# Kernel optimization log

Hardware: AMD Instinct MI355X
Metric: run time of the kernel (lower is better)

Reference implementation:

```python
import jax, jax.numpy as jnp
import numpy as np
import math


def _selective_scan(u, delta, A, Bs, Cs, D, delta_bias):
    """Mamba selective scan.
    u, delta: (B,K,Dn,L); A: (K,Dn,N); Bs, Cs: (B,K,N,L); D, delta_bias: (K,Dn).
    delta_softplus=True semantics from selective_scan_fn.
    """
    delta = jax.nn.softplus(delta + delta_bias[None, :, :, None])
    dl = jnp.moveaxis(delta, -1, 0)  # (L,B,K,Dn)
    ul = jnp.moveaxis(u, -1, 0)      # (L,B,K,Dn)
    bl = jnp.moveaxis(Bs, -1, 0)     # (L,B,K,N)
    cl = jnp.moveaxis(Cs, -1, 0)     # (L,B,K,N)
    h0 = jnp.zeros(u.shape[:3] + (A.shape[-1],), u.dtype)  # (B,K,Dn,N)

    def step(h, inp):
        d, ut, bt, ct = inp
        h = jnp.exp(d[..., None] * A) * h + (d * ut)[..., None] * bt[:, :, None, :]
        y = jnp.einsum('bkdn,bkn->bkd', h, ct)
        return h, y

    _, ys = jax.lax.scan(step, h0, (dl, ul, bl, cl))
    return jnp.moveaxis(ys, 0, -1) + D[None, :, :, None] * u  # (B,K,Dn,L)


def setup_inputs() -> dict:
    key = jax.random.key(0)
    B, H, W, C = 8, 64, 64, 192
    Dn, N, R, K = 192, 8, 12, 4
    ks = jax.random.split(key, 8)
    x = jax.random.normal(ks[0], (B, H, W, C), jnp.float32)
    in_proj_w = jax.random.normal(ks[1], (2 * Dn, C), jnp.float32) * (C ** -0.5)
    conv_w = jax.random.normal(ks[2], (Dn, 1, 3, 3), jnp.float32) * 0.2
    conv_b = jnp.zeros((Dn,), jnp.float32)
    x_proj_w = jax.random.normal(ks[3], (K, R + 2 * N, Dn), jnp.float32) * (Dn ** -0.5)
    dt_std = R ** -0.5
    dt_projs_w = jax.random.uniform(ks[4], (K, Dn, R), jnp.float32, -dt_std, dt_std)
    dt = jnp.exp(jax.random.uniform(ks[5], (K, Dn), jnp.float32)
                 * (math.log(0.1) - math.log(0.001)) + math.log(0.001))
    dt = jnp.clip(dt, 1e-4, None)
    dt_projs_b = dt + jnp.log(-jnp.expm1(-dt))  # inverse softplus
    A_logs = jnp.broadcast_to(jnp.log(jnp.arange(1, N + 1, dtype=jnp.float32)), (K, Dn, N)).copy()
    Ds = jnp.ones((K, Dn), jnp.float32)
    ln_w = jnp.ones((Dn,), jnp.float32)
    ln_b = jnp.zeros((Dn,), jnp.float32)
    out_proj_w = jax.random.normal(ks[6], (C, Dn), jnp.float32) * (Dn ** -0.5)
    return {"x": x, "in_proj_w": in_proj_w, "conv_w": conv_w, "conv_b": conv_b,
            "x_proj_w": x_proj_w, "dt_projs_w": dt_projs_w, "dt_projs_b": dt_projs_b,
            "A_logs": A_logs, "Ds": Ds, "ln_w": ln_w, "ln_b": ln_b,
            "out_proj_w": out_proj_w}


def reference(x, in_proj_w, conv_w, conv_b, x_proj_w, dt_projs_w, dt_projs_b,
              A_logs, Ds, ln_w, ln_b, out_proj_w):
    B, H, W, C = x.shape
    K, _, Dn = x_proj_w.shape
    N = A_logs.shape[-1]
    R = dt_projs_w.shape[-1]
    L = H * W

    xz = x @ in_proj_w.T                       # (B,H,W,2*Dn)
    xf, z = jnp.split(xz, 2, axis=-1)
    xc = jnp.transpose(xf, (0, 3, 1, 2))       # (B,Dn,H,W)
    xc = jax.lax.conv_general_dilated(
        xc, conv_w, (1, 1), [(1, 1), (1, 1)],
        feature_group_count=Dn,
        dimension_numbers=('NCHW', 'OIHW', 'NCHW')) + conv_b[None, :, None, None]
    xc = jax.nn.silu(xc)

    # 4-directional scan sequences: hw, wh, reversed-hw, reversed-wh
    x_hw = xc.reshape(B, Dn, L)
    x_wh = jnp.transpose(xc, (0, 1, 3, 2)).reshape(B, Dn, L)
    x2 = jnp.stack([x_hw, x_wh], axis=1)
    xs = jnp.concatenate([x2, jnp.flip(x2, axis=-1)], axis=1)  # (B,4,Dn,L)

    x_dbl = jnp.einsum('bkdl,kcd->bkcl', xs, x_proj_w)
    dts, Bsx, Csx = jnp.split(x_dbl, [R, R + N], axis=2)
    dts = jnp.einsum('bkrl,kdr->bkdl', dts, dt_projs_w)

    A = -jnp.exp(A_logs)                       # (K,Dn,N)
    out_y = _selective_scan(xs, dts, A, Bsx, Csx, Ds, dt_projs_b)  # (B,4,Dn,L)

    inv_y = jnp.flip(out_y[:, 2:4], axis=-1)
    wh_y = jnp.transpose(out_y[:, 1].reshape(B, Dn, W, H), (0, 1, 3, 2)).reshape(B, Dn, L)
    invwh_y = jnp.transpose(inv_y[:, 1].reshape(B, Dn, W, H), (0, 1, 3, 2)).reshape(B, Dn, L)
    y = out_y[:, 0] + inv_y[:, 0] + wh_y + invwh_y  # (B,Dn,L)

    y = jnp.transpose(y, (0, 2, 1)).reshape(B, H, W, Dn)
    mu = y.mean(-1, keepdims=True)
    var = y.var(-1, keepdims=True)
    y = (y - mu) / jnp.sqrt(var + 1e-5) * ln_w + ln_b
    y = y * jax.nn.silu(z)
    return y @ out_proj_w.T
```

## Files before the change

### kernel.cpp

```cpp
#include <hip/hip_runtime.h>
#include <hip/hip_bf16.h>

constexpr int B_  = 8;
constexpr int H_  = 64;
constexpr int W_  = 64;
constexpr int C_  = 192;
constexpr int Dn  = 192;
constexpr int Nst = 8;
constexpr int R_  = 12;
constexpr int K_  = 4;
constexpr int L_  = H_ * W_;
constexpr int CS  = 32;
constexpr int GS  = 8;
constexpr int NC  = L_ / CS;
constexpr int CPROJ = R_ + 2 * Nst;
constexpr int MROWS = B_ * L_;

typedef __attribute__((ext_vector_type(8))) short short8v;
typedef __attribute__((ext_vector_type(4))) float f32x4;
typedef __attribute__((ext_vector_type(2))) float f32x2;

__device__ __forceinline__ int map_t(int k, int t) {
    int tt = (k >= 2) ? (L_ - 1 - t) : t;
    if (k & 1) tt = (tt & 63) * 64 + (tt >> 6);
    return tt;
}

__device__ __forceinline__ short f2bf(float f) {
    unsigned u = __float_as_uint(f);
    u += 0x7FFFu + ((u >> 16) & 1u);
    return (short)(u >> 16);
}
__device__ __forceinline__ float bf2f(short s) {
    return __uint_as_float(((unsigned)(unsigned short)s) << 16);
}

__device__ __forceinline__ f32x2 mk2(float a, float b) { f32x2 v; v.x = a; v.y = b; return v; }
__device__ __forceinline__ f32x2 lo2(float4 v) { return mk2(v.x, v.y); }
__device__ __forceinline__ f32x2 hi2(float4 v) { return mk2(v.z, v.w); }
__device__ __forceinline__ f32x2 pkfma(f32x2 a, f32x2 b, f32x2 c) {
    return __builtin_elementwise_fma(a, b, c);
}

constexpr int WOFF_IN  = 0;
constexpr int WOFF_XP  = 73728;
constexpr int WOFF_OUT = 95232;
constexpr int WTOTAL   = 132096;
constexpr int XUNITS   = MROWS * Dn / 8;
constexpr int WUNITS   = WTOTAL / 8;
__global__ __launch_bounds__(256) void k_cvt(const float* __restrict__ x,
                                             const float* __restrict__ w_in,
                                             const float* __restrict__ xpw,
                                             const float* __restrict__ wout,
                                             short* __restrict__ x_bf,
                                             short* __restrict__ w_bf) {
    int g = blockIdx.x * 256 + threadIdx.x;
    const float* src;
    short* dst;
    int off;
    if (g < XUNITS) { src = x; dst = x_bf; off = g * 8; }
    else {
        g -= XUNITS;
        if (g >= WUNITS) return;
        int base = g * 8;
        dst = w_bf; off = base;
        if (base < WOFF_XP)       { src = w_in; }
        else if (base < WOFF_OUT) { src = xpw;  src -= WOFF_XP; }
        else                      { src = wout; src -= WOFF_OUT; }
    }
    float4 a = *reinterpret_cast<const float4*>(src + off);
    float4 b = *reinterpret_cast<const float4*>(src + off + 4);
    short8v v = {f2bf(a.x), f2bf(a.y), f2bf(a.z), f2bf(a.w),
                 f2bf(b.x), f2bf(b.y), f2bf(b.z), f2bf(b.w)};
    *reinterpret_cast<short8v*>(dst + off) = v;
}

__device__ __forceinline__ void mgemm_core(const short* __restrict__ A,
                                           const short* __restrict__ Wb,
                                           f32x4 (&acc)[4][2],
                                           int mrow, int ncol, int Nact, int K) {
    const int lane = threadIdx.x & 63;
    const int koff = (lane >> 4) * 8;
    for (int k0 = 0; k0 < K; k0 += 32) {
        short8v af[4], bfr[2];
#pragma unroll
        for (int mf = 0; mf < 4; mf++)
            af[mf] = *reinterpret_cast<const short8v*>(
                A + (size_t)(mrow + mf * 16) * K + k0 + koff);
#pragma unroll
        for (int nf = 0; nf < 2; nf++) {
            int r = ncol + nf * 16;
            short8v z = {0, 0, 0, 0, 0, 0, 0, 0};
            bfr[nf] = (r < Nact)
                ? *reinterpret_cast<const short8v*>(Wb + (size_t)r * K + k0 + koff)
                : z;
        }
#pragma unroll
        for (int mf = 0; mf < 4; mf++)
#pragma unroll
            for (int nf = 0; nf < 2; nf++)
                acc[mf][nf] = __builtin_amdgcn_mfma_f32_16x16x32_bf16(
                    af[mf], bfr[nf], acc[mf][nf], 0, 0, 0);
    }
}

__global__ __launch_bounds__(256) void k_mgemm_f(const short* __restrict__ A,
                                                 const short* __restrict__ Wb,
                                                 float* __restrict__ out0,
                                                 int Nact, int K) {
    const int m0 = blockIdx.x * 128, n0 = blockIdx.y * 64;
    const int wid = threadIdx.x >> 6, lane = threadIdx.x & 63;
    const int wm = wid >> 1, wn = wid & 1;
    f32x4 acc[4][2] = {};
    mgemm_core(A, Wb, acc, m0 + wm * 64 + (lane & 15), n0 + wn * 32 + (lane & 15),
               Nact, K);
    const int prow = (lane >> 4) * 4, pcol = lane & 15;
#pragma unroll
    for (int mf = 0; mf < 4; mf++) {
        int mbase = m0 + wm * 64 + mf * 16 + prow;
#pragma unroll
        for (int nf = 0; nf < 2; nf++) {
            int n = n0 + wn * 32 + nf * 16 + pcol;
            if (n >= Nact) continue;
#pragma unroll
            for (int r = 0; r < 4; r++)
                out0[(size_t)(mbase + r) * Nact + n] = acc[mf][nf][r];
        }
    }
}

__global__ __launch_bounds__(256) void k_mgemm_in(const short* __restrict__ A,
                                                  const short* __restrict__ Wb,
                                                  short* __restrict__ xf_bf,
                                                  short* __restrict__ z_bf,
                                                  int K) {
    const int m0 = blockIdx.x * 128, n0 = blockIdx.y * 64;
    const int wid = threadIdx.x >> 6, lane = threadIdx.x & 63;
    const int wm = wid >> 1, wn = wid & 1;
    f32x4 acc[4][2] = {};
    mgemm_core(A, Wb, acc, m0 + wm * 64 + (lane & 15), n0 + wn * 32 + (lane & 15),
               384, K);
    const int prow = (lane >> 4) * 4, pcol = lane & 15;
#pragma unroll
    for (int mf = 0; mf < 4; mf++) {
        int mbase = m0 + wm * 64 + mf * 16 + prow;
#pragma unroll
        for (int nf = 0; nf < 2; nf++) {
            int n = n0 + wn * 32 + nf * 16 + pcol;
#pragma unroll
            for (int r = 0; r < 4; r++) {
                int m = mbase + r;
                if (n < 192) xf_bf[(size_t)m * 192 + n] = f2bf(acc[mf][nf][r]);
                else         z_bf[(size_t)m * 192 + (n - 192)] = f2bf(acc[mf][nf][r]);
            }
        }
    }
}

__global__ __launch_bounds__(192) void k_conv(const short* __restrict__ xfb,
                                              const float* __restrict__ cw,
                                              const float* __restrict__ cb,
                                              short* __restrict__ xcb) {
    const int tid = threadIdx.x;
    const int dg = tid % 48;
    const int wl = tid / 48;
    const int blk = blockIdx.x;
    const int wq = blk & 15;
    const int hq = (blk >> 4) & 7;
    const int b  = blk >> 7;
    const int w  = wq * 4 + wl;
    const int d  = dg * 4;
    const int h0 = hq * 8;

    short4 win[3][10];
    const short4 z4 = make_short4(0, 0, 0, 0);
#pragma unroll
    for (int kw = 0; kw < 3; kw++) {
        int ww = w + kw - 1;
        bool wok = (unsigned)ww < (unsigned)W_;
        int wc = min(max(ww, 0), W_ - 1);
#pragma unroll
        for (int r = 0; r < 10; r++) {
            int hh = h0 - 1 + r;
            bool ok = wok && ((unsigned)hh < (unsigned)H_);
            int hc = min(max(hh, 0), H_ - 1);
            short4 v = *reinterpret_cast<const short4*>(
                xfb + (((size_t)b * H_ + hc) * W_ + wc) * Dn + d);
            win[kw][r] = ok ? v : z4;
        }
    }

    float wgt[4][9];
    float bias[4];
#pragma unroll
    for (int c = 0; c < 4; c++) {
        bias[c] = cb[d + c];
#pragma unroll
        for (int t = 0; t < 9; t++) wgt[c][t] = cw[(d + c) * 9 + t];
    }

#pragma unroll
    for (int j = 0; j < 8; j++) {
        float a0 = bias[0], a1 = bias[1], a2 = bias[2], a3 = bias[3];
#pragma unroll
        for (int kh = 0; kh < 3; kh++)
#pragma unroll
            for (int kw = 0; kw < 3; kw++) {
                short4 v = win[kw][j + kh];
                int t = kh * 3 + kw;
                a0 = fmaf(bf2f(v.x), wgt[0][t], a0);
                a1 = fmaf(bf2f(v.y), wgt[1][t], a1);
                a2 = fmaf(bf2f(v.z), wgt[2][t], a2);
                a3 = fmaf(bf2f(v.w), wgt[3][t], a3);
            }
        short4 o;
        o.x = f2bf(a0 / (1.f + __expf(-a0)));
        o.y = f2bf(a1 / (1.f + __expf(-a1)));
        o.z = f2bf(a2 / (1.f + __expf(-a2)));
        o.w = f2bf(a3 / (1.f + __expf(-a3)));
        *reinterpret_cast<short4*>(
            xcb + (((size_t)b * H_ + h0 + j) * W_ + w) * Dn + d) = o;
    }
}

__device__ __forceinline__ void delta_e1(float x, float& delta, float& e1) {
    float t = __expf(fminf(x, 80.f));
    float opt = 1.f + t;
    delta = __logf(opt);
    e1 = __builtin_amdgcn_rcpf(opt);
}

__device__ __forceinline__ float dot12p(const float4& q0, const float4& q1,
                                        const float4& q2, const f32x2* w2,
                                        float bias) {
    f32x2 a0 = pkfma(lo2(q0), w2[0], mk2(bias, 0.f));
    f32x2 a1 = lo2(q1) * w2[2];
    a0 = pkfma(hi2(q0), w2[1], a0);
    a1 = pkfma(hi2(q1), w2[3], a1);
    a0 = pkfma(lo2(q2), w2[4], a0);
    a1 = pkfma(hi2(q2), w2[5], a1);
    f32x2 s = a0 + a1;
    return s.x + s.y;
}

__device__ __forceinline__ float dot12(const float4& a, const float4& b,
                                       const float4& c, const float* w, float x) {
    x = fmaf(a.x, w[0], x);  x = fmaf(a.y, w[1], x);
    x = fmaf(a.z, w[2], x);  x = fmaf(a.w, w[3], x);
    x = fmaf(b.x, w[4], x);  x = fmaf(b.y, w[5], x);
    x = fmaf(b.z, w[6], x);  x = fmaf(b.w, w[7], x);
    x = fmaf(c.x, w[8], x);  x = fmaf(c.y, w[9], x);
    x = fmaf(c.z, w[10], x); x = fmaf(c.w, w[11], x);
    return x;
}

__global__ __launch_bounds__(192, 4) void k_scan1(const short* __restrict__ xcb,
                                               const float* __restrict__ xdbl,
                                               const float* __restrict__ dtw_all,
                                               const float* __restrict__ dtb_all,
                                               const float* __restrict__ alog,
                                               float* __restrict__ Aprod,
                                               float* __restrict__ hpart) {
    const int blk = blockIdx.x;
    const int c = blk % NC;
    const int k = (blk / NC) % K_;
    const int b = blk / (NC * K_);
    const int d = threadIdx.x;
    const int t0 = c * CS;
    const int stride = ((k & 1) ? 64 : 1) * ((k >= 2) ? -1 : 1);
    const int lm0 = map_t(k, t0);

    __shared__ float4 sx4[CS][5];
    const float4* xd4 = reinterpret_cast<const float4*>(xdbl);
    for (int i = d; i < CS * 5; i += 192) {
        int ts = i / 5, q = i % 5;
        sx4[ts][q] = xd4[((size_t)b * L_ + lm0 + ts * stride) * 28 + k * 7 + q];
    }
    __syncthreads();

    float dtw[R_];
#pragma unroll
    for (int r = 0; r < R_; r++) dtw[r] = dtw_all[((size_t)k * Dn + d) * R_ + r];
    f32x2 w2[6];
#pragma unroll
    for (int r = 0; r < 6; r++) w2[r] = mk2(dtw[2 * r], dtw[2 * r + 1]);
    const float bias = dtb_all[k * Dn + d];
    float Av[Nst];
    bool fast = true;
#pragma unroll
    for (int n = 0; n < Nst; n++) {
        Av[n] = -__expf(alog[((size_t)k * Dn + d) * Nst + n]);
        fast = fast && (fabsf(Av[n] + (float)(n + 1)) < 1e-3f);
    }

    const long stepD = (long)stride * Dn;
    const short* up = xcb + ((size_t)b * L_ + lm0) * Dn + d;
    size_t base = ((((size_t)(b * K_ + k) * NC + c) * Dn + d)) * Nst;

    if (fast) {
        f32x2 h01 = mk2(0.f, 0.f), h23 = h01, h45 = h01, h67 = h01;
        float p0 = 1.f, p1 = 1.f, p2_ = 1.f, p3_ = 1.f;
        for (int g = 0; g < CS / GS; ++g) {
            const short* ug = up + (long)g * GS * stepD;
            float e1a[GS], dua[GS];
#pragma unroll
            for (int j = 0; j < GS; ++j) {
                int ts = g * GS + j;
                float u = bf2f(ug[(long)j * stepD]);
                float4 q0 = sx4[ts][0], q1 = sx4[ts][1], q2 = sx4[ts][2];
                float delta, e1; delta_e1(dot12p(q0, q1, q2, w2, bias), delta, e1);
                e1a[j] = e1;
                dua[j] = delta * u;
            }
#pragma unroll
            for (int j = 0; j < GS; ++j) {
                int ts = g * GS + j;
                float e1 = e1a[j], du = dua[j];
                float4 qb0 = sx4[ts][3], qb1 = sx4[ts][4];
                float a2 = e1 * e1;
                f32x2 p12 = mk2(e1, a2);
                f32x2 a22 = mk2(a2, a2);
                f32x2 p34 = a22 * p12;
                f32x2 a44 = mk2(p34.y, p34.y);
                f32x2 p56 = a44 * p12;
                f32x2 p78 = a44 * p34;
                f32x2 du2 = mk2(du, du);
                h01 = pkfma(p12, h01, du2 * lo2(qb0));
                h23 = pkfma(p34, h23, du2 * hi2(qb0));
                h45 = pkfma(p56, h45, du2 * lo2(qb1));
                h67 = pkfma(p78, h67, du2 * hi2(qb1));
            }
            p0 *= e1a[0]; p1 *= e1a[1]; p2_ *= e1a[2]; p3_ *= e1a[3];
            p0 *= e1a[4]; p1 *= e1a[5]; p2_ *= e1a[6]; p3_ *= e1a[7];
        }
        float e1p = (p0 * p1) * (p2_ * p3_);
        float p2 = e1p * e1p, p3 = p2 * e1p, p4 = p2 * p2;
        float4* ap4 = reinterpret_cast<float4*>(Aprod + base);
        ap4[0] = make_float4(e1p, p2, p3, p4);
        ap4[1] = make_float4(p4 * e1p, p4 * p2, p4 * p3, p4 * p4);
        float4* hp4 = reinterpret_cast<float4*>(hpart + base);
        hp4[0] = make_float4(h01.x, h01.y, h23.x, h23.y);
        hp4[1] = make_float4(h45.x, h45.y, h67.x, h67.y);
    } else {
        float h[Nst] = {};
        float Ap[Nst];
#pragma unroll
        for (int n = 0; n < Nst; n++) Ap[n] = 1.f;
        float u_next = bf2f(*up);
        const short* upp = up;
        for (int ts = 0; ts < CS; ts++) {
            float u = u_next;
            upp += stepD;
            if (ts + 1 < CS) u_next = bf2f(*upp);
            float4 q0 = sx4[ts][0], q1 = sx4[ts][1], q2 = sx4[ts][2];
            float4 qb0 = sx4[ts][3], qb1 = sx4[ts][4];
            float Bv[Nst] = {qb0.x, qb0.y, qb0.z, qb0.w, qb1.x, qb1.y, qb1.z, qb1.w};
            float delta, e1; delta_e1(dot12(q0, q1, q2, dtw, bias), delta, e1);
            float du = delta * u;
#pragma unroll
            for (int n = 0; n < Nst; n++) {
                float a = __expf(delta * Av[n]);
                Ap[n] *= a;
                h[n] = fmaf(a, h[n], du * Bv[n]);
            }
        }
#pragma unroll
        for (int n = 0; n < Nst; n++) { Aprod[base + n] = Ap[n]; hpart[base + n] = h[n]; }
    }
}

__global__ __launch_bounds__(256) void k_scan2(const float* __restrict__ Aprod,
                                               const float* __restrict__ hpart,
                                               float* __restrict__ hin) {
    int idx = blockIdx.x * 256 + threadIdx.x;
    int dn = idx % (Dn * Nst);
    int bk = idx / (Dn * Nst);
    size_t stride = (size_t)Dn * Nst;
    size_t base = (size_t)bk * NC * stride + dn;
    float h = 0.f;
    for (int cc = 0; cc < NC; cc++) {
        size_t s = base + (size_t)cc * stride;
        hin[s] = h;
        h = fmaf(Aprod[s], h, hpart[s]);
    }
}

__global__ __launch_bounds__(192, 4) void k_scan3(const short* __restrict__ xcb,
                                               const float* __restrict__ xdbl,
                                               const float* __restrict__ dtw_all,
                                               const float* __restrict__ dtb_all,
                                               const float* __restrict__ alog,
                                               const float* __restrict__ dvec,
                                               const float* __restrict__ hin,
                                               short* __restrict__ y0,
                                               short* __restrict__ y1,
                                               short* __restrict__ y2,
                                               short* __restrict__ y3) {
    const int blk = blockIdx.x;
    const int c = blk % NC;
    const int k = (blk / NC) % K_;
    const int b = blk / (NC * K_);
    const int d = threadIdx.x;
    const int t0 = c * CS;
    const int stride = ((k & 1) ? 64 : 1) * ((k >= 2) ? -1 : 1);
    const int lm0 = map_t(k, t0);
    short* __restrict__ yk = (k == 0) ? y0 : (k == 1) ? y1 : (k == 2) ? y2 : y3;

    __shared__ float4 sx4[CS][7];
    const float4* xd4 = reinterpret_cast<const float4*>(xdbl);
    for (int i = d; i < CS * 7; i += 192) {
        int ts = i / 7, q = i % 7;
        sx4[ts][q] = xd4[((size_t)b * L_ + lm0 + ts * stride) * 28 + k * 7 + q];
    }
    __syncthreads();

    float dtw[R_];
#pragma unroll
    for (int r = 0; r < R_; r++) dtw[r] = dtw_all[((size_t)k * Dn + d) * R_ + r];
    f32x2 w2[6];
#pragma unroll
    for (int r = 0; r < 6; r++) w2[r] = mk2(dtw[2 * r], dtw[2 * r + 1]);
    const float bias = dtb_all[k * Dn + d];
    const float Dk = dvec[k * Dn + d];
    float Av[Nst];
    bool fast = true;
#pragma unroll
    for (int n = 0; n < Nst; n++) {
        Av[n] = -__expf(alog[((size_t)k * Dn + d) * Nst + n]);
        fast = fast && (fabsf(Av[n] + (float)(n + 1)) < 1e-3f);
    }

    size_t hbase = ((((size_t)(b * K_ + k) * NC + c) * Dn + d)) * Nst;
    const long stepD = (long)stride * Dn;
    const short* up = xcb + ((size_t)b * L_ + lm0) * Dn + d;
    short* yp = yk + ((size_t)b * L_ + lm0) * Dn + d;

    if (fast) {
        const float4* hi4 = reinterpret_cast<const float4*>(hin + hbase);
        float4 ha = hi4[0], hb = hi4[1];
        f32x2 h01 = lo2(ha), h23 = hi2(ha), h45 = lo2(hb), h67 = hi2(hb);
        for (int g = 0; g < CS / GS; ++g) {
            const short* ug = up + (long)g * GS * stepD;
            short* yg = yp + (long)g * GS * stepD;
            float e1a[GS], dua[GS], dku[GS];
#pragma unroll
            for (int j = 0; j < GS; ++j) {
                int ts = g * GS + j;
                float u = bf2f(ug[(long)j * stepD]);
                float4 q0 = sx4[ts][0], q1 = sx4[ts][1], q2 = sx4[ts][2];
                float delta, e1; delta_e1(dot12p(q0, q1, q2, w2, bias), delta, e1);
                e1a[j] = e1;
                dua[j] = delta * u;
                dku[j] = Dk * u;
            }
#pragma unroll
            for (int j = 0; j < GS; ++j) {
                int ts = g * GS + j;
                float e1 = e1a[j], du = dua[j];
                float4 qb0 = sx4[ts][3], qb1 = sx4[ts][4];
                float4 qc0 = sx4[ts][5], qc1 = sx4[ts][6];
                float a2 = e1 * e1;
                f32x2 p12 = mk2(e1, a2);
                f32x2 a22 = mk2(a2, a2);
                f32x2 p34 = a22 * p12;
                f32x2 a44 = mk2(p34.y, p34.y);
                f32x2 p56 = a44 * p12;
                f32x2 p78 = a44 * p34;
                f32x2 du2 = mk2(du, du);
                h01 = pkfma(p12, h01, du2 * lo2(qb0));
                h23 = pkfma(p34, h23, du2 * hi2(qb0));
                h45 = pkfma(p56, h45, du2 * lo2(qb1));
                h67 = pkfma(p78, h67, du2 * hi2(qb1));
                f32x2 yacc = mk2(dku[j], 0.f);
                yacc = pkfma(h01, lo2(qc0), yacc);
                yacc = pkfma(h23, hi2(qc0), yacc);
                yacc = pkfma(h45, lo2(qc1), yacc);
                yacc = pkfma(h67, hi2(qc1), yacc);
                yg[(long)j * stepD] = f2bf(yacc.x + yacc.y);
            }
        }
    } else {
        float h[Nst];
#pragma unroll
        for (int n = 0; n < Nst; n++) h[n] = hin[hbase + n];
        float u_next = bf2f(*up);
        const short* upp = up;
        short* ypp = yp;
        for (int ts = 0; ts < CS; ts++) {
            float u = u_next;
            upp += stepD;
            if (ts + 1 < CS) u_next = bf2f(*upp);
            float4 q0 = sx4[ts][0], q1 = sx4[ts][1], q2 = sx4[ts][2];
            float4 qb0 = sx4[ts][3], qb1 = sx4[ts][4];
            float4 qc0 = sx4[ts][5], qc1 = sx4[ts][6];
            float Bv[Nst] = {qb0.x, qb0.y, qb0.z, qb0.w, qb1.x, qb1.y, qb1.z, qb1.w};
            float Cv[Nst] = {qc0.x, qc0.y, qc0.z, qc0.w, qc1.x, qc1.y, qc1.z, qc1.w};
            float delta, e1; delta_e1(dot12(q0, q1, q2, dtw, bias), delta, e1);
            float du = delta * u;
            float y = Dk * u;
#pragma unroll
            for (int n = 0; n < Nst; n++) {
                float a = __expf(delta * Av[n]);
                h[n] = fmaf(a, h[n], du * Bv[n]);
                y = fmaf(h[n], Cv[n], y);
            }
            *ypp = f2bf(y);
            ypp += stepD;
        }
    }
}

__global__ __launch_bounds__(256) void k_ln(const short* __restrict__ y0,
                                            const short* __restrict__ y1,
                                            const short* __restrict__ y2,
                                            const short* __restrict__ y3,
                                            const short* __restrict__ zb,
                                            const float* __restrict__ lnw,
                                            const float* __restrict__ lnb,
                                            short* __restrict__ yfin) {
    const int row = blockIdx.x * 4 + (threadIdx.x >> 6);
    const int lane = threadIdx.x & 63;
    const size_t base = (size_t)row * Dn;
    float v[3];
    float s = 0.f, s2 = 0.f;
#pragma unroll
    for (int j = 0; j < 3; j++) {
        size_t idx = base + lane + j * 64;
        v[j] = bf2f(y0[idx]) + bf2f(y1[idx]) + bf2f(y2[idx]) + bf2f(y3[idx]);
        s += v[j];
        s2 = fmaf(v[j], v[j], s2);
    }
#pragma unroll
    for (int o = 1; o < 64; o <<= 1) {
        s += __shfl_xor(s, o);
        s2 += __shfl_xor(s2, o);
    }
    const float inv = 1.f / 192.f;
    float mu = s * inv;
    float var = s2 * inv - mu * mu;
    float rstd = rsqrtf(var + 1e-5f);
#pragma unroll
    for (int j = 0; j < 3; j++) {
        int dd = lane + j * 64;
        size_t idx = base + dd;
        float zz = bf2f(zb[idx]);
        float sig = 1.f / (1.f + __expf(-zz));
        float res = ((v[j] - mu) * rstd * lnw[dd] + lnb[dd]) * (zz * sig);
        yfin[idx] = f2bf(res);
    }
}

extern "C" void kernel_launch(void* const* d_in, const int* in_sizes, int n_in,
                              void* d_out, int out_size, void* d_ws, size_t ws_size,
                              hipStream_t stream) {
    const float* x    = (const float*)d_in[0];
    const float* w_in = (const float*)d_in[1];
    const float* cw   = (const float*)d_in[2];
    const float* cb   = (const float*)d_in[3];
    const float* xpw  = (const float*)d_in[4];
    const float* dtw  = (const float*)d_in[5];
    const float* dtb  = (const float*)d_in[6];
    const float* alog = (const float*)d_in[7];
    const float* dvec = (const float*)d_in[8];
    const float* lnw  = (const float*)d_in[9];
    const float* lnb  = (const float*)d_in[10];
    const float* wout = (const float*)d_in[11];
    float* out = (float*)d_out;

    const size_t SH  = (size_t)MROWS * Dn;
    const size_t SCN = (size_t)B_ * K_ * NC * Dn * Nst;

    char* p = (char*)d_ws;
    short* x_bf  = (short*)p; p += SH * 2;
    short* xf_bf = (short*)p; p += SH * 2;
    short* z_bf  = (short*)p; p += SH * 2;
    short* xc_bf = (short*)p; p += SH * 2;
    float* xdbl  = (float*)p; p += (size_t)MROWS * (K_ * CPROJ) * 4;
    float* Aprod = (float*)p; p += SCN * 4;
    float* hpart = (float*)p; p += SCN * 4;
    float* hin   = (float*)p; p += SCN * 4;
    short* w_bf  = (short*)p;
    short* y0 = x_bf;
    short* y1 = xf_bf;
    short* y2 = (short*)Aprod;
    short* y3 = (short*)hpart;
    short* yfin_bf = (short*)hin;

    k_cvt<<<(XUNITS + WUNITS + 255) / 256, 256, 0, stream>>>(x, w_in, xpw, wout,
                                                             x_bf, w_bf);
    k_mgemm_in<<<dim3(MROWS / 128, 6), 256, 0, stream>>>(x_bf, w_bf + WOFF_IN,
                                                         xf_bf, z_bf, C_);
    k_conv<<<B_ * (H_ / 8) * (W_ / 4), 192, 0, stream>>>(xf_bf, cw, cb, xc_bf);
    k_mgemm_f<<<dim3(MROWS / 128, 2), 256, 0, stream>>>(xc_bf, w_bf + WOFF_XP,
                                                        xdbl, K_ * CPROJ, Dn);
    k_scan1<<<B_ * K_ * NC, 192, 0, stream>>>(xc_bf, xdbl, dtw, dtb, alog, Aprod, hpart);
    k_scan2<<<(B_ * K_ * Dn * Nst) / 256, 256, 0, stream>>>(Aprod, hpart, hin);
    k_scan3<<<B_ * K_ * NC, 192, 0, stream>>>(xc_bf, xdbl, dtw, dtb, alog, dvec,
                                              hin, y0, y1, y2, y3);
    k_ln<<<MROWS / 4, 256, 0, stream>>>(y0, y1, y2, y3, z_bf, lnw, lnb, yfin_bf);
    k_mgemm_f<<<dim3(MROWS / 128, 3), 256, 0, stream>>>(yfin_bf, w_bf + WOFF_OUT,
                                                        out, C_, Dn);
}
```

Baseline: 201.6 us.

## Process two independent scan chunks per block for ILP in scan kernels

After: 228.8 us. +13.5%, slower.

```diff
diff --git a/kernel.cpp b/kernel.cpp
--- a/kernel.cpp
+++ b/kernel.cpp
@@ -11,8 +11,8 @@
 constexpr int K_  = 4;
 constexpr int L_  = H_ * W_;
 constexpr int CS  = 32;
-constexpr int GS  = 8;
 constexpr int NC  = L_ / CS;
+constexpr int NCP = NC / 2;
 constexpr int CPROJ = R_ + 2 * Nst;
 constexpr int MROWS = B_ * L_;
 
@@ -40,6 +40,23 @@
 __device__ __forceinline__ f32x2 hi2(float4 v) { return mk2(v.z, v.w); }
 __device__ __forceinline__ f32x2 pkfma(f32x2 a, f32x2 b, f32x2 c) {
     return __builtin_elementwise_fma(a, b, c);
+}
+
+__device__ __forceinline__ void hstep(f32x2& h01, f32x2& h23, f32x2& h45,
+                                      f32x2& h67, float e1, float du,
+                                      float4 qb0, float4 qb1) {
+    float a2 = e1 * e1;
+    f32x2 p12 = mk2(e1, a2);
+    f32x2 a22 = mk2(a2, a2);
+    f32x2 p34 = a22 * p12;
+    f32x2 a44 = mk2(p34.y, p34.y);
+    f32x2 p56 = a44 * p12;
+    f32x2 p78 = a44 * p34;
+    f32x2 du2 = mk2(du, du);
+    h01 = pkfma(p12, h01, du2 * lo2(qb0));
+    h23 = pkfma(p34, h23, du2 * hi2(qb0));
+    h45 = pkfma(p56, h45, du2 * lo2(qb1));
+    h67 = pkfma(p78, h67, du2 * hi2(qb1));
 }
 
 constexpr int WOFF_IN  = 0;
@@ -262,17 +279,17 @@
                                                float* __restrict__ Aprod,
                                                float* __restrict__ hpart) {
     const int blk = blockIdx.x;
-    const int c = blk % NC;
-    const int k = (blk / NC) % K_;
-    const int b = blk / (NC * K_);
+    const int cp = blk % NCP;
+    const int k = (blk / NCP) % K_;
+    const int b = blk / (NCP * K_);
     const int d = threadIdx.x;
-    const int t0 = c * CS;
+    const int t0 = cp * 64;
     const int stride = ((k & 1) ? 64 : 1) * ((k >= 2) ? -1 : 1);
     const int lm0 = map_t(k, t0);
 
-    __shared__ float4 sx4[CS][5];
+    __shared__ float4 sx4[64][5];
     const float4* xd4 = reinterpret_cast<const float4*>(xdbl);
-    for (int i = d; i < CS * 5; i += 192) {
+    for (int i = d; i < 64 * 5; i += 192) {
         int ts = i / 5, q = i % 5;
         sx4[ts][q] = xd4[((size_t)b * L_ + lm0 + ts * stride) * 28 + k * 7 + q];
     }
@@ -295,77 +312,81 @@
 
     const long stepD = (long)stride * Dn;
     const short* up = xcb + ((size_t)b * L_ + lm0) * Dn + d;
-    size_t base = ((((size_t)(b * K_ + k) * NC + c) * Dn + d)) * Nst;
+    const size_t baseA = ((((size_t)(b * K_ + k) * NC + 2 * cp) * Dn + d)) * Nst;
+    const size_t baseB = baseA + (size_t)Dn * Nst;
 
     if (fast) {
-        f32x2 h01 = mk2(0.f, 0.f), h23 = h01, h45 = h01, h67 = h01;
-        float p0 = 1.f, p1 = 1.f, p2_ = 1.f, p3_ = 1.f;
-        for (int g = 0; g < CS / GS; ++g) {
-            const short* ug = up + (long)g * GS * stepD;
-            float e1a[GS], dua[GS];
-#pragma unroll
-            for (int j = 0; j < GS; ++j) {
-                int ts = g * GS + j;
-                float u = bf2f(ug[(long)j * stepD]);
+        f32x2 hA01 = mk2(0.f, 0.f), hA23 = hA01, hA45 = hA01, hA67 = hA01;
+        f32x2 hB01 = hA01, hB23 = hA01, hB45 = hA01, hB67 = hA01;
+        float pA0 = 1.f, pA1 = 1.f, pA2 = 1.f, pA3 = 1.f;
+        float pB0 = 1.f, pB1 = 1.f, pB2 = 1.f, pB3 = 1.f;
+        for (int g = 0; g < 8; ++g) {
+            float e1A[4], duA[4], e1B[4], duB[4];
+#pragma unroll
+            for (int j = 0; j < 4; ++j) {
+                int tA = g * 4 + j, tB = tA + 32;
+                float uA = bf2f(up[(long)tA * stepD]);
+                float uB = bf2f(up[(long)tB * stepD]);
+                float dA, eA, dB, eB;
+                delta_e1(dot12p(sx4[tA][0], sx4[tA][1], sx4[tA][2], w2, bias), dA, eA);
+                delta_e1(dot12p(sx4[tB][0], sx4[tB][1], sx4[tB][2], w2, bias), dB, eB);
+                e1A[j] = eA; duA[j] = dA * uA;
+                e1B[j] = eB; duB[j] = dB * uB;
+            }
+#pragma unroll
+            for (int j = 0; j < 4; ++j) {
+                int tA = g * 4 + j, tB = tA + 32;
+                hstep(hA01, hA23, hA45, hA67, e1A[j], duA[j], sx4[tA][3], sx4[tA][4]);
+                hstep(hB01, hB23, hB45, hB67, e1B[j], duB[j], sx4[tB][3], sx4[tB][4]);
+            }
+            pA0 *= e1A[0]; pA1 *= e1A[1]; pA2 *= e1A[2]; pA3 *= e1A[3];
+            pB0 *= e1B[0]; pB1 *= e1B[1]; pB2 *= e1B[2]; pB3 *= e1B[3];
+        }
+        float eA = (pA0 * pA1) * (pA2 * pA3);
+        float eB = (pB0 * pB1) * (pB2 * pB3);
+        {
+            float p2 = eA * eA, p3 = p2 * eA, p4 = p2 * p2;
+            float4* ap4 = reinterpret_cast<float4*>(Aprod + baseA);
+            ap4[0] = make_float4(eA, p2, p3, p4);
+            ap4[1] = make_float4(p4 * eA, p4 * p2, p4 * p3, p4 * p4);
+            float4* hp4 = reinterpret_cast<float4*>(hpart + baseA);
+            hp4[0] = make_float4(hA01.x, hA01.y, hA23.x, hA23.y);
+            hp4[1] = make_float4(hA45.x, hA45.y, hA67.x, hA67.y);
+        }
+        {
+            float p2 = eB * eB, p3 = p2 * eB, p4 = p2 * p2;
+            float4* ap4 = reinterpret_cast<float4*>(Aprod + baseB);
+            ap4[0] = make_float4(eB, p2, p3, p4);
+            ap4[1] = make_float4(p4 * eB, p4 * p2, p4 * p3, p4 * p4);
+            float4* hp4 = reinterpret_cast<float4*>(hpart + baseB);
+            hp4[0] = make_float4(hB01.x, hB01.y, hB23.x, hB23.y);
+            hp4[1] = make_float4(hB45.x, hB45.y, hB67.x, hB67.y);
+        }
+    } else {
+#pragma unroll
+        for (int half = 0; half < 2; ++half) {
+            float h[Nst] = {};
+            float Ap[Nst];
+#pragma unroll
+            for (int n = 0; n < Nst; n++) Ap[n] = 1.f;
+            for (int ts = half * 32; ts < half * 32 + 32; ts++) {
+                float u = bf2f(up[(long)ts * stepD]);
                 float4 q0 = sx4[ts][0], q1 = sx4[ts][1], q2 = sx4[ts][2];
-                float delta, e1; delta_e1(dot12p(q0, q1, q2, w2, bias), delta, e1);
-                e1a[j] = e1;
-                dua[j] = delta * u;
-            }
-#pragma unroll
-            for (int j = 0; j < GS; ++j) {
-                int ts = g * GS + j;
-                float e1 = e1a[j], du = dua[j];
                 float4 qb0 = sx4[ts][3], qb1 = sx4[ts][4];
-                float a2 = e1 * e1;
-                f32x2 p12 = mk2(e1, a2);
-                f32x2 a22 = mk2(a2, a2);
-                f32x2 p34 = a22 * p12;
-                f32x2 a44 = mk2(p34.y, p34.y);
-                f32x2 p56 = a44 * p12;
-                f32x2 p78 = a44 * p34;
-                f32x2 du2 = mk2(du, du);
-                h01 = pkfma(p12, h01, du2 * lo2(qb0));
-                h23 = pkfma(p34, h23, du2 * hi2(qb0));
-                h45 = pkfma(p56, h45, du2 * lo2(qb1));
-                h67 = pkfma(p78, h67, du2 * hi2(qb1));
-            }
-            p0 *= e1a[0]; p1 *= e1a[1]; p2_ *= e1a[2]; p3_ *= e1a[3];
-            p0 *= e1a[4]; p1 *= e1a[5]; p2_ *= e1a[6]; p3_ *= e1a[7];
-        }
-        float e1p = (p0 * p1) * (p2_ * p3_);
-        float p2 = e1p * e1p, p3 = p2 * e1p, p4 = p2 * p2;
-        float4* ap4 = reinterpret_cast<float4*>(Aprod + base);
-        ap4[0] = make_float4(e1p, p2, p3, p4);
-        ap4[1] = make_float4(p4 * e1p, p4 * p2, p4 * p3, p4 * p4);
-        float4* hp4 = reinterpret_cast<float4*>(hpart + base);
-        hp4[0] = make_float4(h01.x, h01.y, h23.x, h23.y);
-        hp4[1] = make_float4(h45.x, h45.y, h67.x, h67.y);
-    } else {
-        float h[Nst] = {};
-        float Ap[Nst];
-#pragma unroll
-        for (int n = 0; n < Nst; n++) Ap[n] = 1.f;
-        float u_next = bf2f(*up);
-        const short* upp = up;
-        for (int ts = 0; ts < CS; ts++) {
-            float u = u_next;
-            upp += stepD;
-            if (ts + 1 < CS) u_next = bf2f(*upp);
-            float4 q0 = sx4[ts][0], q1 = sx4[ts][1], q2 = sx4[ts][2];
-            float4 qb0 = sx4[ts][3], qb1 = sx4[ts][4];
-            float Bv[Nst] = {qb0.x, qb0.y, qb0.z, qb0.w, qb1.x, qb1.y, qb1.z, qb1.w};
-            float delta, e1; delta_e1(dot12(q0, q1, q2, dtw, bias), delta, e1);
-            float du = delta * u;
-#pragma unroll
-            for (int n = 0; n < Nst; n++) {
-                float a = __expf(delta * Av[n]);
-                Ap[n] *= a;
-                h[n] = fmaf(a, h[n], du * Bv[n]);
-            }
-        }
-#pragma unroll
-        for (int n = 0; n < Nst; n++) { Aprod[base + n] = Ap[n]; hpart[base + n] = h[n]; }
+                float Bv[Nst] = {qb0.x, qb0.y, qb0.z, qb0.w, qb1.x, qb1.y, qb1.z, qb1.w};
+                float delta, e1; delta_e1(dot12(q0, q1, q2, dtw, bias), delta, e1);
+                float du = delta * u;
+#pragma unroll
+                for (int n = 0; n < Nst; n++) {
+                    float a = __expf(delta * Av[n]);
+                    Ap[n] *= a;
+                    h[n] = fmaf(a, h[n], du * Bv[n]);
+                }
+            }
+            size_t base = half ? baseB : baseA;
+#pragma unroll
+            for (int n = 0; n < Nst; n++) { Aprod[base + n] = Ap[n]; hpart[base + n] = h[n]; }
+        }
     }
 }
 
@@ -397,18 +418,18 @@
                                                short* __restrict__ y2,
                                                short* __restrict__ y3) {
     const int blk = blockIdx.x;
-    const int c = blk % NC;
-    const int k = (blk / NC) % K_;
-    const int b = blk / (NC * K_);
+    const int cp = blk % NCP;
+    const int k = (blk / NCP) % K_;
+    const int b = blk / (NCP * K_);
     const int d = threadIdx.x;
-    const int t0 = c * CS;
+    const int t0 = cp * 64;
     const int stride = ((k & 1) ? 64 : 1) * ((k >= 2) ? -1 : 1);
     const int lm0 = map_t(k, t0);
     short* __restrict__ yk = (k == 0) ? y0 : (k == 1) ? y1 : (k == 2) ? y2 : y3;
 
-    __shared__ float4 sx4[CS][7];
+    __shared__ float4 sx4[64][7];
     const float4* xd4 = reinterpret_cast<const float4*>(xdbl);
-    for (int i = d; i < CS * 7; i += 192) {
+    for (int i = d; i < 64 * 7; i += 192) {
         int ts = i / 7, q = i % 7;
         sx4[ts][q] = xd4[((size_t)b * L_ + lm0 + ts * stride) * 28 + k * 7 + q];
     }
@@ -430,82 +451,75 @@
         fast = fast && (fabsf(Av[n] + (float)(n + 1)) < 1e-3f);
     }
 
-    size_t hbase = ((((size_t)(b * K_ + k) * NC + c) * Dn + d)) * Nst;
+    const size_t baseA = ((((size_t)(b * K_ + k) * NC + 2 * cp) * Dn + d)) * Nst;
+    const size_t baseB = baseA + (size_t)Dn * Nst;
     const long stepD = (long)stride * Dn;
     const short* up = xcb + ((size_t)b * L_ + lm0) * Dn + d;
     short* yp = yk + ((size_t)b * L_ + lm0) * Dn + d;
 
     if (fast) {
-        const float4* hi4 = reinterpret_cast<const float4*>(hin + hbase);
-        float4 ha = hi4[0], hb = hi4[1];
-        f32x2 h01 = lo2(ha), h23 = hi2(ha), h45 = lo2(hb), h67 = hi2(hb);
-        for (int g = 0; g < CS / GS; ++g) {
-            const short* ug = up + (long)g * GS * stepD;
-            short* yg = yp + (long)g * GS * stepD;
-            float e1a[GS], dua[GS], dku[GS];
-#pragma unroll
-            for (int j = 0; j < GS; ++j) {
-                int ts = g * GS + j;
-                float u = bf2f(ug[(long)j * stepD]);
+        const float4* hiA = reinterpret_cast<const float4*>(hin + baseA);
+        const float4* hiB = reinterpret_cast<const float4*>(hin + baseB);
+        float4 ha = hiA[0], hb = hiA[1], hc = hiB[0], hd = hiB[1];
+        f32x2 hA01 = lo2(ha), hA23 = hi2(ha), hA45 = lo2(hb), hA67 = hi2(hb);
+        f32x2 hB01 = lo2(hc), hB23 = hi2(hc), hB45 = lo2(hd), hB67 = hi2(hd);
+        for (int g = 0; g < 8; ++g) {
+            float e1A[4], duA[4], dkA[4], e1B[4], duB[4], dkB[4];
+#pragma unroll
+            for (int j = 0; j < 4; ++j) {
+                int tA = g * 4 + j, tB = tA + 32;
+                float uA = bf2f(up[(long)tA * stepD]);
+                float uB = bf2f(up[(long)tB * stepD]);
+                float dA, eA, dB, eB;
+                delta_e1(dot12p(sx4[tA][0], sx4[tA][1], sx4[tA][2], w2, bias), dA, eA);
+                delta_e1(dot12p(sx4[tB][0], sx4[tB][1], sx4[tB][2], w2, bias), dB, eB);
+                e1A[j] = eA; duA[j] = dA * uA; dkA[j] = Dk * uA;
+                e1B[j] = eB; duB[j] = dB * uB; dkB[j] = Dk * uB;
+            }
+#pragma unroll
+            for (int j = 0; j < 4; ++j) {
+                int tA = g * 4 + j, tB = tA + 32;
+                hstep(hA01, hA23, hA45, hA67, e1A[j], duA[j], sx4[tA][3], sx4[tA][4]);
+                f32x2 ya = mk2(dkA[j], 0.f);
+                ya = pkfma(hA01, lo2(sx4[tA][5]), ya);
+                ya = pkfma(hA23, hi2(sx4[tA][5]), ya);
+                ya = pkfma(hA45, lo2(sx4[tA][6]), ya);
+                ya = pkfma(hA67, hi2(sx4[tA][6]), ya);
+                yp[(long)tA * stepD] = f2bf(ya.x + ya.y);
+                hstep(hB01, hB23, hB45, hB67, e1B[j], duB[j], sx4[tB][3], sx4[tB][4]);
+                f32x2 yb = mk2(dkB[j], 0.f);
+                yb = pkfma(hB01, lo2(sx4[tB][5]), yb);
+                yb = pkfma(hB23, hi2(sx4[tB][5]), yb);
+                yb = pkfma(hB45, lo2(sx4[tB][6]), yb);
+                yb = pkfma(hB67, hi2(sx4[tB][6]), yb);
+                yp[(long)tB * stepD] = f2bf(yb.x + yb.y);
+            }
+        }
+    } else {
+#pragma unroll
+        for (int half = 0; half < 2; ++half) {
+            size_t hbase = half ? baseB : baseA;
+            float h[Nst];
+#pragma unroll
+            for (int n = 0; n < Nst; n++) h[n] = hin[hbase + n];
+            for (int ts = half * 32; ts < half * 32 + 32; ts++) {
+                float u = bf2f(up[(long)ts * stepD]);
                 float4 q0 = sx4[ts][0], q1 = sx4[ts][1], q2 = sx4[ts][2];
-                float delta, e1; delta_e1(dot12p(q0, q1, q2, w2, bias), delta, e1);
-                e1a[j] = e1;
-                dua[j] = delta * u;
-                dku[j] = Dk * u;
-            }
-#pragma unroll
-            for (int j = 0; j < GS; ++j) {
-                int ts = g * GS + j;
-                float e1 = e1a[j], du = dua[j];
                 float4 qb0 = sx4[ts][3], qb1 = sx4[ts][4];
                 float4 qc0 = sx4[ts][5], qc1 = sx4[ts][6];
-                float a2 = e1 * e1;
-                f32x2 p12 = mk2(e1, a2);
-                f32x2 a22 = mk2(a2, a2);
-                f32x2 p34 = a22 * p12;
-                f32x2 a44 = mk2(p34.y, p34.y);
-                f32x2 p56 = a44 * p12;
-                f32x2 p78 = a44 * p34;
-                f32x2 du2 = mk2(du, du);
-                h01 = pkfma(p12, h01, du2 * lo2(qb0));
-                h23 = pkfma(p34, h23, du2 * hi2(qb0));
-                h45 = pkfma(p56, h45, du2 * lo2(qb1));
-                h67 = pkfma(p78, h67, du2 * hi2(qb1));
-                f32x2 yacc = mk2(dku[j], 0.f);
-                yacc = pkfma(h01, lo2(qc0), yacc);
-                yacc = pkfma(h23, hi2(qc0), yacc);
-                yacc = pkfma(h45, lo2(qc1), yacc);
-                yacc = pkfma(h67, hi2(qc1), yacc);
-                yg[(long)j * stepD] = f2bf(yacc.x + yacc.y);
-            }
-        }
-    } else {
-        float h[Nst];
-#pragma unroll
-        for (int n = 0; n < Nst; n++) h[n] = hin[hbase + n];
-        float u_next = bf2f(*up);
-        const short* upp = up;
-        short* ypp = yp;
-        for (int ts = 0; ts < CS; ts++) {
-            float u = u_next;
-            upp += stepD;
-            if (ts + 1 < CS) u_next = bf2f(*upp);
-            float4 q0 = sx4[ts][0], q1 = sx4[ts][1], q2 = sx4[ts][2];
-            float4 qb0 = sx4[ts][3], qb1 = sx4[ts][4];
-            float4 qc0 = sx4[ts][5], qc1 = sx4[ts][6];
-            float Bv[Nst] = {qb0.x, qb0.y, qb0.z, qb0.w, qb1.x, qb1.y, qb1.z, qb1.w};
-            float Cv[Nst] = {qc0.x, qc0.y, qc0.z, qc0.w, qc1.x, qc1.y, qc1.z, qc1.w};
-            float delta, e1; delta_e1(dot12(q0, q1, q2, dtw, bias), delta, e1);
-            float du = delta * u;
-            float y = Dk * u;
-#pragma unroll
-            for (int n = 0; n < Nst; n++) {
-                float a = __expf(delta * Av[n]);
-                h[n] = fmaf(a, h[n], du * Bv[n]);
-                y = fmaf(h[n], Cv[n], y);
-            }
-            *ypp = f2bf(y);
-            ypp += stepD;
+                float Bv[Nst] = {qb0.x, qb0.y, qb0.z, qb0.w, qb1.x, qb1.y, qb1.z, qb1.w};
+                float Cv[Nst] = {qc0.x, qc0.y, qc0.z, qc0.w, qc1.x, qc1.y, qc1.z, qc1.w};
+                float delta, e1; delta_e1(dot12(q0, q1, q2, dtw, bias), delta, e1);
+                float du = delta * u;
+                float y = Dk * u;
+#pragma unroll
+                for (int n = 0; n < Nst; n++) {
+                    float a = __expf(delta * Av[n]);
+                    h[n] = fmaf(a, h[n], du * Bv[n]);
+                    y = fmaf(h[n], Cv[n], y);
+                }
+                yp[(long)ts * stepD] = f2bf(y);
+            }
         }
     }
 }
@@ -593,10 +607,11 @@
     k_conv<<<B_ * (H_ / 8) * (W_ / 4), 192, 0, stream>>>(xf_bf, cw, cb, xc_bf);
     k_mgemm_f<<<dim3(MROWS / 128, 2), 256, 0, stream>>>(xc_bf, w_bf + WOFF_XP,
                                                         xdbl, K_ * CPROJ, Dn);
-    k_scan1<<<B_ * K_ * NC, 192, 0, stream>>>(xc_bf, xdbl, dtw, dtb, alog, Aprod, hpart);
+    k_scan1<<<B_ * K_ * NCP, 192, 0, stream>>>(xc_bf, xdbl, dtw, dtb, alog,
+                                               Aprod, hpart);
     k_scan2<<<(B_ * K_ * Dn * Nst) / 256, 256, 0, stream>>>(Aprod, hpart, hin);
-    k_scan3<<<B_ * K_ * NC, 192, 0, stream>>>(xc_bf, xdbl, dtw, dtb, alog, dvec,
-                                              hin, y0, y1, y2, y3);
+    k_scan3<<<B_ * K_ * NCP, 192, 0, stream>>>(xc_bf, xdbl, dtw, dtb, alog, dvec,
+                                               hin, y0, y1, y2, y3);
     k_ln<<<MROWS / 4, 256, 0, stream>>>(y0, y1, y2, y3, z_bf, lnw, lnb, yfin_bf);
     k_mgemm_f<<<dim3(MROWS / 128, 3), 256, 0, stream>>>(yfin_bf, w_bf + WOFF_OUT,
                                                         out, C_, Dn);
```
